# Optimization experiments

Measured on AMD Instinct MI355X. Metric: run time of the kernel, lower is better.

Reference implementation:

```python
import jax, jax.numpy as jnp
import numpy as np

B, T, W = 8, 4096, 1024          # batch, byte seq len, words per sequence
DB, DW = 64, 512                 # byte_embed_dim, word_embed_dim
NH = 2                           # highway layers per block
VOCAB = 264                      # 256 bytes + 4 + 4 specials
BPE_MARK, WORD_MARK = 4, 3       # bpe_mask_idx, word_mask_idx


def _make_seg_ids():
    # ragged word lengths in {3,4,5}, mean 4, summing to T per sequence
    rng = np.random.default_rng(0)
    seg = np.empty((B, T), np.int32)
    base = T // W
    for b in range(B):
        delta = np.zeros(W, np.int64)
        q = W // 4
        idx = rng.permutation(W)
        delta[idx[:q]] = 1
        delta[idx[q:2 * q]] = -1
        seg[b] = np.repeat(np.arange(W), base + delta)
    return jnp.asarray(seg)


def setup_inputs() -> dict:
    key = jax.random.key(0)
    ks = jax.random.split(key, 12)
    s = 0.05
    byte_tokens = jax.random.randint(ks[0], (B, T), 4, VOCAB)
    bpe_mask = jax.random.bernoulli(ks[1], 0.25, (B, T))
    word_mask = jax.random.bernoulli(ks[2], 0.05, (B, T))
    seg_ids = _make_seg_ids()
    tok_emb = (jax.random.normal(ks[3], (VOCAB, DB)) * s).at[0].set(0.0)  # padding_idx=0 row zeroed
    inp = {
        'byte_tokens': byte_tokens, 'bpe_mask': bpe_mask, 'word_mask': word_mask,
        'seg_ids': seg_ids, 'tok_emb': tok_emb,
        'conv0_w': jax.random.normal(ks[4], (3, DB, DW)) * s, 'conv0_b': jnp.zeros((DW,)),
        'hw0_wg': jax.random.normal(ks[5], (NH, DW, DW)) * s, 'hw0_bg': jnp.zeros((NH, DW)),
        'hw0_wh': jax.random.normal(ks[6], (NH, DW, DW)) * s, 'hw0_bh': jnp.zeros((NH, DW)),
        'conv1_w': jax.random.normal(ks[7], (3, DW, DW)) * s, 'conv1_b': jnp.zeros((DW,)),
        'hw1_wg': jax.random.normal(ks[8], (NH, DW, DW)) * s, 'hw1_bg': jnp.zeros((NH, DW)),
        'hw1_wh': jax.random.normal(ks[9], (NH, DW, DW)) * s, 'hw1_bh': jnp.zeros((NH, DW)),
        'proj_w': jax.random.normal(ks[10], (DW, DW)) * s, 'proj_b': jnp.zeros((DW,)),
    }
    return inp


def _conv_highway(x, cw, cb, wg, bg, wh, bh, residual):
    # 1D same-padded conv over sequence, optional residual, relu, then highways
    y = jax.lax.conv_general_dilated(x, cw, (1,), 'SAME',
                                     dimension_numbers=('NWC', 'WIO', 'NWC')) + cb
    if residual:
        y = y + x
    y = jax.nn.relu(y)
    for i in range(NH):
        g = jax.nn.sigmoid(y @ wg[i] + bg[i])
        h = jax.nn.relu(y @ wh[i] + bh[i])
        y = g * h + (1.0 - g) * y
    return y


def reference(byte_tokens, bpe_mask, word_mask, seg_ids, tok_emb,
              conv0_w, conv0_b, hw0_wg, hw0_bg, hw0_wh, hw0_bh,
              conv1_w, conv1_b, hw1_wg, hw1_bg, hw1_wh, hw1_bh,
              proj_w, proj_b):
    # byte embedding + marker embeddings (pad idx 0 -> zero row)
    x = (tok_emb[byte_tokens]
         + tok_emb[jnp.where(bpe_mask, BPE_MARK, 0)]
         + tok_emb[jnp.where(word_mask, WORD_MARK, 0)])          # [B,T,DB]
    x = _conv_highway(x, conv0_w, conv0_b, hw0_wg, hw0_bg, hw0_wh, hw0_bh, False)
    x = _conv_highway(x, conv1_w, conv1_b, hw1_wg, hw1_bg, hw1_wh, hw1_bh, True)
    # ragged per-word segment max over bytes (fused, replaces python loops)
    seg_max = jax.vmap(lambda xi, si: jax.ops.segment_max(xi, si, num_segments=W))
    x = seg_max(x, seg_ids)                                       # [B,W,DW]
    return x @ proj_w + proj_b
```

## Files before the change

kernel.cpp:

```cpp
#include <hip/hip_runtime.h>
#include <hip/hip_bf16.h>

using bf16 = __hip_bfloat16;
typedef __attribute__((ext_vector_type(8))) short s8v;
typedef __attribute__((ext_vector_type(4))) float f4v;

#define T_SEQ 4096
#define DWC 512

__device__ __forceinline__ float fin(float v) {
    return (v == v && fabsf(v) < 1e30f) ? v : 0.0f;
}
__device__ __forceinline__ float ldf(const void* p, size_t i, int f32) {
    return f32 ? ((const float*)p)[i] : __bfloat162float(((const bf16*)p)[i]);
}
__device__ __forceinline__ float b2f(short s) {
    unsigned u = ((unsigned)(unsigned short)s) << 16;
    return __builtin_bit_cast(float, u);
}
__device__ __forceinline__ short f2b(float v) {
    bf16 b = __float2bfloat16(v);
    return __builtin_bit_cast(short, b);
}
__device__ __forceinline__ uint4 ld16(const short* p) { return *(const uint4*)p; }

__device__ __forceinline__ void gl_lds16(const short* g, short* l) {
    __builtin_amdgcn_global_load_lds(
        (const __attribute__((address_space(1))) void*)g,
        (__attribute__((address_space(3))) void*)l, 16, 0, 0);
}

__device__ __forceinline__ void swz(int L, int G, int& bx, int& by) {
    int k8 = L & 7, sl = L >> 3;
    int gp = G >> 5;
    bx = sl & 3;
    by = k8 * gp + (sl >> 2);
}

__device__ __forceinline__ int swidx(int row, int ch) {
    return row * 32 + ((ch ^ ((row >> 1) & 3)) << 3);
}

__global__ __launch_bounds__(256) void diag_kernel(bf16* __restrict__ out, int n, float v)
{
    int i = blockIdx.x * 256 + threadIdx.x;
    if (i < n) out[i] = __float2bfloat16(i == 0 ? v : 0.0f);
}

__global__ __launch_bounds__(256) void detect_kernel(
    const int* __restrict__ tok, const unsigned char* __restrict__ bpe,
    const unsigned char* __restrict__ wm, const int* __restrict__ seg,
    const unsigned int* __restrict__ embw, int* __restrict__ flags)
{
    __shared__ int sh[5];
    int tid = threadIdx.x;
    if (tid < 5) sh[tid] = 0;
    __syncthreads();
    int bo = 0, bm = 0, wo = 0, wmid = 0;
    for (int i = tid; i < 16384; i += 256) {
        int odd = 2 * i + 1;
        if (bpe[odd]) bo = 1;
        if (wm[odd])  wo = 1;
        int mid = 8 * (i & 4095) + 4;
        if (bpe[mid]) bm = 1;
        if (wm[mid])  wmid = 1;
    }
    if (bo)   atomicOr(&sh[0], 1);
    if (bm)   atomicOr(&sh[1], 1);
    if (wo)   atomicOr(&sh[2], 1);
    if (wmid) atomicOr(&sh[3], 1);
    if (tid < 32 && embw[32 + tid] != 0u) atomicOr(&sh[4], 1);
    __syncthreads();
    if (tid == 0) {
        flags[0] = (tok[32767] != 0) ? 0 : 1;
        flags[1] = sh[0] ? 1 : (sh[1] ? 4 : 8);
        flags[2] = sh[2] ? 1 : (sh[3] ? 4 : 8);
        flags[3] = (seg[32767] != 0) ? 0 : 1;
        flags[4] = sh[4] ? 0 : 1;
    }
}

#define WB_TOTAL 3249664
#define EMB4_ELEMS (264 * 4 * 64)
__global__ __launch_bounds__(256) void convert_weights(
    const void* c0w, const void* c0b, const void* h0g, const void* h0bg,
    const void* h0h, const void* h0bh, const void* c1w, const void* c1b,
    const void* h1g, const void* h1bg, const void* h1h, const void* h1bh,
    const void* pw, const void* pb, const void* emb,
    const int* __restrict__ flags, short* __restrict__ WB)
{
    int f32 = flags[4];
    size_t i = (size_t)blockIdx.x * 256 + threadIdx.x;
    if (i >= WB_TOTAL + EMB4_ELEMS) return;
    if (i >= WB_TOTAL) {
        size_t o = i - WB_TOTAL;
        size_t t = o >> 8, v = (o >> 6) & 3, c = o & 63;
        float val = ldf(emb, t * 64 + c, f32);
        if (v & 1) val += ldf(emb, 4 * 64 + c, f32);
        if (v & 2) val += ldf(emb, 3 * 64 + c, f32);
        WB[i] = f2b(fin(val));
        return;
    }
    const void* src; size_t si;
    auto fraginv = [](size_t r, size_t& k, size_t& n) {
        size_t blk = r >> 9, w = r & 511;
        n = (blk >> 4) * 16 + ((w >> 3) & 15);
        k = (blk & 15) * 32 + (w >> 7) * 8 + (w & 7);
    };
    if (i < 98304)        { size_t n = i / 192, k = i % 192; src = c0w; si = k * 512 + n; }
    else if (i < 98816)   { src = c0b;  si = i - 98304; }
    else if (i < 623104)  { size_t o = i - 98816;  size_t l = o >> 18; size_t k, n;
                            fraginv(o & 262143, k, n);
                            src = h0g; si = (l << 18) + k * 512 + n; }
    else if (i < 624128)  { src = h0bg; si = i - 623104; }
    else if (i < 1148416) { size_t o = i - 624128; size_t l = o >> 18; size_t k, n;
                            fraginv(o & 262143, k, n);
                            src = h0h; si = (l << 18) + k * 512 + n; }
    else if (i < 1149440) { src = h0bh; si = i - 1148416; }
    else if (i < 1935872) { size_t o = i - 1149440; size_t n = o / 1536, k = o % 1536;
                            src = c1w; si = k * 512 + n; }
    else if (i < 1936384) { src = c1b;  si = i - 1935872; }
    else if (i < 2460672) { size_t o = i - 1936384; size_t l = o >> 18; size_t k, n;
                            fraginv(o & 262143, k, n);
                            src = h1g; si = (l << 18) + k * 512 + n; }
    else if (i < 2461696) { src = h1bg; si = i - 2460672; }
    else if (i < 2985984) { size_t o = i - 2461696; size_t l = o >> 18; size_t k, n;
                            fraginv(o & 262143, k, n);
                            src = h1h; si = (l << 18) + k * 512 + n; }
    else if (i < 2987008) { src = h1bh; si = i - 2985984; }
    else if (i < 3249152) { size_t o = i - 2987008; size_t n = o >> 9, k = o & 511;
                            src = pw; si = k * 512 + n; }
    else                  { src = pb;   si = i - 3249152; }
    WB[i] = f2b(ldf(src, si, f32));
}

__global__ __launch_bounds__(512) void conv0_mfma(
    const int* __restrict__ tok, const unsigned char* __restrict__ bpe,
    const unsigned char* __restrict__ wm, const short* __restrict__ emb4,
    const int* __restrict__ flags, const short* __restrict__ WT,
    const short* __restrict__ bias, short* __restrict__ Out)
{
    constexpr int K = 192;
    constexpr int NIT = 3;
    __shared__ __align__(16) short As[2][256 * 32];
    __shared__ __align__(16) short Bs[2][256 * 32];
    int bx, by;
    swz(blockIdx.x, gridDim.x, bx, by);
    const int bm = by * 128, bn = bx * 128;
    const int tid = threadIdx.x;
    const int wave = tid >> 6, lane = tid & 63;
    const int wmr = (wave >> 1) * 32, wnc = (wave & 1) * 64;
    const int q = lane >> 4, ln16 = lane & 15;
    const int sr = tid >> 2, sch = tid & 3;
    const int tt = (bm + sr) & (T_SEQ - 1);
    const int is64t = flags[0];
    const int wb = flags[1], ww = flags[2];
    const short* Bb = WT + (size_t)(bn + sr) * K + sch * 8;

    f4v acc[2][4] = {};
    uint4 rA0, rA1, rB0, rB1;
    const uint4 z4 = make_uint4(0, 0, 0, 0);

    auto loadA = [&](int tap, uint4& a0, uint4& a1) {
        int ts = tt + tap - 1;
        if ((unsigned)ts < (unsigned)T_SEQ) {
            int bt = bm + sr + tap - 1;
            int tk = is64t ? (int)((const long long*)tok)[bt] : tok[bt];
            tk = min(max(tk, 0), 263);
            int v = (bpe[(size_t)bt * wb] ? 1 : 0) | (wm[(size_t)bt * ww] ? 2 : 0);
            const short* row = emb4 + ((size_t)tk * 4 + v) * 64;
            a0 = ld16(row + sch * 8);
            a1 = ld16(row + 32 + sch * 8);
        } else { a0 = z4; a1 = z4; }
    };

    loadA(0, rA0, rA1);
    rB0 = ld16(Bb);
    rB1 = ld16(Bb + 32);
    *(uint4*)(&As[0][swidx(sr, sch)])       = rA0;
    *(uint4*)(&As[0][swidx(128 + sr, sch)]) = rA1;
    *(uint4*)(&Bs[0][swidx(sr, sch)])       = rB0;
    *(uint4*)(&Bs[0][swidx(128 + sr, sch)]) = rB1;
    __syncthreads();
    int p = 0;

    for (int it = 0; it < NIT; ++it) {
        const bool more = (it + 1 < NIT);
        if (more) {
            int kn = (it + 1) * 64;
            loadA(it + 1, rA0, rA1);
            rB0 = ld16(Bb + kn);
            rB1 = ld16(Bb + kn + 32);
        }
        #pragma unroll
        for (int ks = 0; ks < 2; ks++) {
            s8v af[2], bf[4];
            #pragma unroll
            for (int mi = 0; mi < 2; mi++)
                af[mi] = *(const s8v*)(&As[p][swidx(128 * ks + wmr + mi * 16 + ln16, q)]);
            #pragma unroll
            for (int ni = 0; ni < 4; ni++)
                bf[ni] = *(const s8v*)(&Bs[p][swidx(128 * ks + wnc + ni * 16 + ln16, q)]);
            #pragma unroll
            for (int mi = 0; mi < 2; mi++)
                #pragma unroll
                for (int ni = 0; ni < 4; ni++)
                    acc[mi][ni] = __builtin_amdgcn_mfma_f32_16x16x32_bf16(
                        af[mi], bf[ni], acc[mi][ni], 0, 0, 0);
        }
        if (more) {
            *(uint4*)(&As[p ^ 1][swidx(sr, sch)])       = rA0;
            *(uint4*)(&As[p ^ 1][swidx(128 + sr, sch)]) = rA1;
            *(uint4*)(&Bs[p ^ 1][swidx(sr, sch)])       = rB0;
            *(uint4*)(&Bs[p ^ 1][swidx(128 + sr, sch)]) = rB1;
            __syncthreads();
            p ^= 1;
        }
    }

    #pragma unroll
    for (int mi = 0; mi < 2; mi++)
        #pragma unroll
        for (int ni = 0; ni < 4; ni++) {
            int col = bn + wnc + ni * 16 + ln16;
            float bv = b2f(bias[col]);
            #pragma unroll
            for (int r = 0; r < 4; r++) {
                int orow = bm + wmr + mi * 16 + q * 4 + r;
                Out[(size_t)orow * DWC + col] =
                    f2b(fin(fmaxf(acc[mi][ni][r] + bv, 0.0f)));
            }
        }
}

__global__ __launch_bounds__(512) void conv1_mfma(
    const short* __restrict__ A, const short* __restrict__ WT,
    const short* __restrict__ bias, short* __restrict__ Out)
{
    constexpr int IC = 512;
    constexpr int K = 3 * IC;
    constexpr int NIT = K / 64;
    __shared__ __align__(16) short As[2][256 * 32];
    __shared__ __align__(16) short Bs[2][256 * 32];
    int bx, by;
    swz(blockIdx.x, gridDim.x, bx, by);
    const int bm = by * 128, bn = bx * 128;
    const int tid = threadIdx.x;
    const int wave = tid >> 6, lane = tid & 63;
    const int wmr = (wave >> 1) * 32, wnc = (wave & 1) * 64;
    const int q = lane >> 4, ln16 = lane & 15;
    const int sr = tid >> 2, sch = tid & 3;
    const int tt = (bm + sr) & (T_SEQ - 1);
    const short* Bb = WT + (size_t)(bn + sr) * K + sch * 8;

    f4v acc[2][4] = {};
    uint4 rA0, rA1, rB0, rB1;
    const uint4 z4 = make_uint4(0, 0, 0, 0);

    {
        int ts = tt - 1;
        bool ok = (ts >= 0 && ts < T_SEQ);
        const short* sa = A + (size_t)(bm + sr - 1) * IC + sch * 8;
        rA0 = ok ? ld16(sa) : z4;
        rA1 = ok ? ld16(sa + 32) : z4;
        rB0 = ld16(Bb);
        rB1 = ld16(Bb + 32);
    }
    *(uint4*)(&As[0][swidx(sr, sch)])       = rA0;
    *(uint4*)(&As[0][swidx(128 + sr, sch)]) = rA1;
    *(uint4*)(&Bs[0][swidx(sr, sch)])       = rB0;
    *(uint4*)(&Bs[0][swidx(128 + sr, sch)]) = rB1;
    __syncthreads();
    int p = 0;

    for (int it = 0; it < NIT; ++it) {
        const bool more = (it + 1 < NIT);
        if (more) {
            int kn = (it + 1) * 64;
            int tap = kn / IC, c0 = kn - tap * IC;
            int ts = tt + tap - 1;
            bool ok = (ts >= 0 && ts < T_SEQ);
            const short* sa = A + (size_t)(bm + sr + tap - 1) * IC + c0 + sch * 8;
            rA0 = ok ? ld16(sa) : z4;
            rA1 = ok ? ld16(sa + 32) : z4;
            rB0 = ld16(Bb + kn);
            rB1 = ld16(Bb + kn + 32);
        }
        #pragma unroll
        for (int ks = 0; ks < 2; ks++) {
            s8v af[2], bf[4];
            #pragma unroll
            for (int mi = 0; mi < 2; mi++)
                af[mi] = *(const s8v*)(&As[p][swidx(128 * ks + wmr + mi * 16 + ln16, q)]);
            #pragma unroll
            for (int ni = 0; ni < 4; ni++)
                bf[ni] = *(const s8v*)(&Bs[p][swidx(128 * ks + wnc + ni * 16 + ln16, q)]);
            #pragma unroll
            for (int mi = 0; mi < 2; mi++)
                #pragma unroll
                for (int ni = 0; ni < 4; ni++)
                    acc[mi][ni] = __builtin_amdgcn_mfma_f32_16x16x32_bf16(
                        af[mi], bf[ni], acc[mi][ni], 0, 0, 0);
        }
        if (more) {
            *(uint4*)(&As[p ^ 1][swidx(sr, sch)])       = rA0;
            *(uint4*)(&As[p ^ 1][swidx(128 + sr, sch)]) = rA1;
            *(uint4*)(&Bs[p ^ 1][swidx(sr, sch)])       = rB0;
            *(uint4*)(&Bs[p ^ 1][swidx(128 + sr, sch)]) = rB1;
            __syncthreads();
            p ^= 1;
        }
    }

    #pragma unroll
    for (int mi = 0; mi < 2; mi++)
        #pragma unroll
        for (int ni = 0; ni < 4; ni++) {
            int col = bn + wnc + ni * 16 + ln16;
            float bv = b2f(bias[col]);
            #pragma unroll
            for (int r = 0; r < 4; r++) {
                int orow = bm + wmr + mi * 16 + q * 4 + r;
                float v = acc[mi][ni][r] + bv + b2f(A[(size_t)orow * IC + col]);
                Out[(size_t)orow * DWC + col] = f2b(fin(fmaxf(v, 0.0f)));
            }
        }
}

__global__ __launch_bounds__(512, 4) void highway_mfma8(
    const short* __restrict__ Y, const short* __restrict__ WgF,
    const short* __restrict__ bg, const short* __restrict__ WhF,
    const short* __restrict__ bh, short* __restrict__ Out)
{
    constexpr int IC = DWC;
    constexpr int NIT = IC / 32;
    __shared__ __align__(16) short L[3][128 * 32];
    int bx, by;
    swz(blockIdx.x, gridDim.x, bx, by);
    const int bm = by * 128, bn = bx * 128;
    const int tid = threadIdx.x;
    const int wave = tid >> 6, lane = tid & 63;
    const int wmr = (wave >> 2) * 64;
    const int wnc = (wave & 3) * 32;
    const int q = lane >> 4, ln16 = lane & 15;

    const int rr = (wave << 4) + (lane >> 2);
    const int ch = (lane & 3) ^ ((rr >> 1) & 3);
    const short* gA = Y + (size_t)(bm + rr) * IC + ch * 8;
    const int wb1k = wave << 10;

    const short* Bg0 = WgF + (((size_t)(bn + wnc) >> 4) << 13) + (lane << 3);
    const short* Bh0 = WhF + (((size_t)(bn + wnc) >> 4) << 13) + (lane << 3);

    f4v accg[4][2] = {};
    f4v acch[4][2] = {};

    auto stage = [&](int pp, int kk) {
        gl_lds16(gA + kk, (short*)((char*)&L[pp][0] + wb1k));
    };

    stage(0, 0);
    stage(1, 32);
    asm volatile("s_waitcnt vmcnt(1)" ::: "memory");
    __builtin_amdgcn_s_barrier();
    int cur = 0, nn = 2;

    for (int it = 0; it < NIT; ++it) {
        const bool issue = (it + 2 < NIT);
        s8v bgf[2], bhf[2];
        #pragma unroll
        for (int ni = 0; ni < 2; ni++) {
            size_t fo = ((size_t)ni << 13) + ((size_t)it << 9);
            bgf[ni] = *(const s8v*)(Bg0 + fo);
            bhf[ni] = *(const s8v*)(Bh0 + fo);
        }
        if (issue) stage(nn, (it + 2) * 32);
        const short* Ap = &L[cur][0];
        s8v af[2];
        #pragma unroll
        for (int mh = 0; mh < 2; mh++) {
            #pragma unroll
            for (int mi = 0; mi < 2; mi++)
                af[mi] = *(const s8v*)(&Ap[swidx(wmr + mh * 32 + mi * 16 + ln16, q)]);
            #pragma unroll
            for (int mi = 0; mi < 2; mi++)
                #pragma unroll
                for (int ni = 0; ni < 2; ni++) {
                    accg[mh * 2 + mi][ni] = __builtin_amdgcn_mfma_f32_16x16x32_bf16(
                        af[mi], bgf[ni], accg[mh * 2 + mi][ni], 0, 0, 0);
                    acch[mh * 2 + mi][ni] = __builtin_amdgcn_mfma_f32_16x16x32_bf16(
                        af[mi], bhf[ni], acch[mh * 2 + mi][ni], 0, 0, 0);
                }
        }
        if (it + 1 < NIT) {
            if (issue) asm volatile("s_waitcnt vmcnt(1)" ::: "memory");
            else       asm volatile("s_waitcnt vmcnt(0)" ::: "memory");
            __builtin_amdgcn_s_barrier();
            cur = (cur == 2) ? 0 : cur + 1;
            nn  = (nn  == 2) ? 0 : nn  + 1;
        }
    }

    #pragma unroll
    for (int mi = 0; mi < 4; mi++)
        #pragma unroll
        for (int ni = 0; ni < 2; ni++) {
            int col = bn + wnc + ni * 16 + ln16;
            float bgv = b2f(bg[col]);
            float bhv = b2f(bh[col]);
            #pragma unroll
            for (int r = 0; r < 4; r++) {
                int orow = bm + wmr + mi * 16 + q * 4 + r;
                float g = 1.0f / (1.0f + expf(-(accg[mi][ni][r] + bgv)));
                float h = fmaxf(acch[mi][ni][r] + bhv, 0.0f);
                float yv = b2f(Y[(size_t)orow * DWC + col]);
                Out[(size_t)orow * DWC + col] = f2b(fin(g * h + (1.0f - g) * yv));
            }
        }
}

__global__ __launch_bounds__(512) void proj_mfma(
    const short* __restrict__ A, const short* __restrict__ WT,
    const short* __restrict__ bias, const int* __restrict__ flags,
    void* __restrict__ Out, int oroff)
{
    __shared__ __align__(16) short As[128 * 32];
    __shared__ __align__(16) short Bs[128 * 32];
    int bx, by;
    swz(blockIdx.x, gridDim.x, bx, by);
    const int bm = by * 128, bn = bx * 128;
    const int tid = threadIdx.x;
    const int wave = tid >> 6, lane = tid & 63;
    const int wmr = (wave >> 1) * 32, wnc = (wave & 1) * 64;
    const int q = lane >> 4, ln16 = lane & 15;
    const int sr = tid >> 2, sch = tid & 3;
    const int sw = swidx(sr, sch);
    const int f32 = flags[4];
    const short* A0 = A  + (size_t)(bm + sr) * DWC + sch * 8;
    const short* B0 = WT + (size_t)(bn + sr) * DWC + sch * 8;

    f4v acc[2][4] = {};
    uint4 rA = ld16(A0), rB = ld16(B0);

    for (int k0 = 0; k0 < DWC; k0 += 32) {
        *(uint4*)(&As[sw]) = rA;
        *(uint4*)(&Bs[sw]) = rB;
        __syncthreads();
        if (k0 + 32 < DWC) {
            int kn = k0 + 32;
            rA = ld16(A0 + kn); rB = ld16(B0 + kn);
        }
        s8v af[2], bf[4];
        #pragma unroll
        for (int mi = 0; mi < 2; mi++) af[mi] = *(const s8v*)(&As[swidx(wmr + mi * 16 + ln16, q)]);
        #pragma unroll
        for (int ni = 0; ni < 4; ni++) bf[ni] = *(const s8v*)(&Bs[swidx(wnc + ni * 16 + ln16, q)]);
        #pragma unroll
        for (int mi = 0; mi < 2; mi++)
            #pragma unroll
            for (int ni = 0; ni < 4; ni++)
                acc[mi][ni] = __builtin_amdgcn_mfma_f32_16x16x32_bf16(
                    af[mi], bf[ni], acc[mi][ni], 0, 0, 0);
        __syncthreads();
    }

    #pragma unroll
    for (int mi = 0; mi < 2; mi++)
        #pragma unroll
        for (int ni = 0; ni < 4; ni++) {
            int col = bn + wnc + ni * 16 + ln16;
            float bv = b2f(bias[col]);
            #pragma unroll
            for (int r = 0; r < 4; r++) {
                int orow = bm + wmr + mi * 16 + q * 4 + r;
                float v = fin(acc[mi][ni][r] + bv);
                size_t oi = (size_t)(oroff + orow) * DWC + col;
                if (f32) ((float*)Out)[oi] = v;
                else     ((bf16*)Out)[oi] = __float2bfloat16(v);
            }
        }
}

__global__ __launch_bounds__(256) void bounds_kernel(
    const int* __restrict__ seg, const int* __restrict__ flags,
    int* __restrict__ wstart, int* __restrict__ wend, int bt0)
{
    int il = blockIdx.x * 256 + threadIdx.x;
    int ig = bt0 + il;
    int is64 = flags[3];
    const long long* seg64 = (const long long*)seg;
    int t = il & (T_SEQ - 1);
    int bl = il >> 12;
    int s  = (is64 ? (int)seg64[ig] : seg[ig]) & 1023;
    int sp = (t == 0)         ? -1 : ((is64 ? (int)seg64[ig - 1] : seg[ig - 1]) & 1023);
    int sn = (t == T_SEQ - 1) ? -1 : ((is64 ? (int)seg64[ig + 1] : seg[ig + 1]) & 1023);
    int bw = (bl << 10) + s;
    if (sp != s) wstart[bw] = t;
    if (sn != s) wend[bw] = t;
}

__global__ __launch_bounds__(512) void segmax_kernel(
    const short* __restrict__ Y, const int* __restrict__ wstart,
    const int* __restrict__ wend, short* __restrict__ Out)
{
    int bw = blockIdx.x;
    int d = threadIdx.x;
    int bl = bw >> 10;
    int s = wstart[bw], e = wend[bw];
    s = min(max(s, 0), T_SEQ - 1);
    e = min(max(e, s), T_SEQ - 1);
    float m = b2f(Y[(size_t)((bl << 12) + s) * DWC + d]);
    for (int t = s + 1; t <= e; ++t)
        m = fmaxf(m, b2f(Y[(size_t)((bl << 12) + t) * DWC + d]));
    Out[(size_t)bw * DWC + d] = f2b(fin(m));
}

extern "C" void kernel_launch(void* const* d_in, const int* in_sizes, int n_in,
                              void* d_out, int out_size, void* d_ws, size_t ws_size,
                              hipStream_t stream)
{
    static const int expect[19] = {32768, 32768, 32768, 32768, 16896,
                                   98304, 512, 524288, 1024, 524288, 1024,
                                   786432, 512, 524288, 1024, 524288, 1024,
                                   262144, 512};
    int bad = -1;
    if (n_in < 19) bad = 31;
    else for (int i = 0; i < 19; i++) if (in_sizes[i] != expect[i]) { bad = i; break; }
    if (bad >= 0) {
        diag_kernel<<<dim3((out_size + 255) / 256), dim3(256), 0, stream>>>(
            (bf16*)d_out, out_size, 1e35f * (float)(1 + bad));
        return;
    }

    char* ws = (char*)d_ws;
    const size_t WBREG = 8ull << 20;
    short* WB    = (short*)ws;
    int*   flags = (int*)(ws + (7u << 20));
    const size_t perC = 8388608 + 8192 + 64;
    int C = 8;
    while (C > 1 && WBREG + (size_t)C * perC > ws_size) C >>= 1;
    if (WBREG + (size_t)C * perC > ws_size) {
        float ws_mib = (float)((double)ws_size / 1048576.0);
        diag_kernel<<<dim3((out_size + 255) / 256), dim3(256), 0, stream>>>(
            (bf16*)d_out, out_size, 1e30f * (16.0f + ws_mib));
        return;
    }

    const int*  byte_tokens = (const int*)d_in[0];
    const unsigned char* bpe_mask = (const unsigned char*)d_in[1];
    const unsigned char* word_mask = (const unsigned char*)d_in[2];
    const int*  seg_ids     = (const int*)d_in[3];
    const void* tok_emb = d_in[4];

    detect_kernel<<<dim3(1), dim3(256), 0, stream>>>(
        byte_tokens, bpe_mask, word_mask, seg_ids,
        (const unsigned int*)tok_emb, flags);

    convert_weights<<<dim3((WB_TOTAL + EMB4_ELEMS + 255) / 256), dim3(256), 0, stream>>>(
        d_in[5], d_in[6], d_in[7], d_in[8], d_in[9], d_in[10],
        d_in[11], d_in[12], d_in[13], d_in[14], d_in[15], d_in[16],
        d_in[17], d_in[18], tok_emb, flags, WB);

    short* c0wT = WB;            short* c0b  = WB + 98304;
    short* h0gF = WB + 98816;    short* h0bg = WB + 623104;
    short* h0hF = WB + 624128;   short* h0bh = WB + 1148416;
    short* c1wT = WB + 1149440;  short* c1b  = WB + 1935872;
    short* h1gF = WB + 1936384;  short* h1bg = WB + 2460672;
    short* h1hF = WB + 2461696;  short* h1bh = WB + 2985984;
    short* pwT  = WB + 2987008;  short* pb   = WB + 3249152;
    short* emb4 = WB + WB_TOTAL;
    const int LOFF = 262144, LBOFF = 512;

    for (int b0 = 0; b0 < 8; b0 += C) {
        const int rows  = C * T_SEQ;
        const int words = C * 1024;
        char*  chunk  = ws + WBREG;
        short* U      = (short*)chunk;
        short* V      = (short*)(chunk + (size_t)C * 4194304);
        int*   wstart = (int*)(chunk + (size_t)C * 8388608);
        int*   wend   = wstart + words;
        short* segout = U;

        dim3 gg(4 * (rows / 128));
        conv0_mfma<<<gg, dim3(512), 0, stream>>>(
            byte_tokens + (size_t)b0 * T_SEQ,
            bpe_mask, word_mask, emb4, flags, c0wT, c0b, U);

        highway_mfma8<<<gg, dim3(512), 0, stream>>>(U, h0gF, h0bg, h0hF, h0bh, V);
        highway_mfma8<<<gg, dim3(512), 0, stream>>>(V, h0gF + LOFF, h0bg + LBOFF,
                                                    h0hF + LOFF, h0bh + LBOFF, U);

        conv1_mfma<<<gg, dim3(512), 0, stream>>>(U, c1wT, c1b, V);

        highway_mfma8<<<gg, dim3(512), 0, stream>>>(V, h1gF, h1bg, h1hF, h1bh, U);
        highway_mfma8<<<gg, dim3(512), 0, stream>>>(U, h1gF + LOFF, h1bg + LBOFF,
                                                    h1hF + LOFF, h1bh + LBOFF, V);

        bounds_kernel<<<dim3(rows / 256), dim3(256), 0, stream>>>(
            seg_ids, flags, wstart, wend, b0 * T_SEQ);

        segmax_kernel<<<dim3(words), dim3(512), 0, stream>>>(V, wstart, wend, segout);

        proj_mfma<<<dim3(4 * (words / 128)), dim3(512), 0, stream>>>(
            segout, pwT, pb, flags, d_out, b0 * 1024);
    }
}
```

Baseline: 414.6 us.

## Tile weight conversion through LDS and stash highway residual tiles for coalesced output

```diff
diff --git a/kernel.cpp b/kernel.cpp
--- a/kernel.cpp
+++ b/kernel.cpp
@@ -82,56 +82,78 @@
 
 #define WB_TOTAL 3249664
 #define EMB4_ELEMS (264 * 4 * 64)
-__global__ __launch_bounds__(256) void convert_weights(
-    const void* c0w, const void* c0b, const void* h0g, const void* h0bg,
-    const void* h0h, const void* h0bh, const void* c1w, const void* c1b,
-    const void* h1g, const void* h1bg, const void* h1h, const void* h1bh,
-    const void* pw, const void* pb, const void* emb,
+
+__global__ __launch_bounds__(256) void convert_mats(
+    const void* c0w, const void* h0g, const void* h0h, const void* c1w,
+    const void* h1g, const void* h1h, const void* pw,
     const int* __restrict__ flags, short* __restrict__ WB)
 {
-    int f32 = flags[4];
-    size_t i = (size_t)blockIdx.x * 256 + threadIdx.x;
-    if (i >= WB_TOTAL + EMB4_ELEMS) return;
-    if (i >= WB_TOTAL) {
-        size_t o = i - WB_TOTAL;
-        size_t t = o >> 8, v = (o >> 6) & 3, c = o & 63;
-        float val = ldf(emb, t * 64 + c, f32);
+    __shared__ short lds[64][66];
+    const int f32 = flags[4];
+    const int bid = blockIdx.x;
+    const void* src; size_t soff, dbase; int K, t; bool frag;
+    if (bid < 24)       { src = c0w; soff = 0; dbase = 0;       K = 192;  frag = false; t = bid; }
+    else if (bid < 152) { int b = bid - 24;  int l = b >> 6; t = b & 63;
+                          src = h0g; soff = (size_t)l << 18; dbase = 98816   + ((size_t)l << 18); K = 512; frag = true; }
+    else if (bid < 280) { int b = bid - 152; int l = b >> 6; t = b & 63;
+                          src = h0h; soff = (size_t)l << 18; dbase = 624128  + ((size_t)l << 18); K = 512; frag = true; }
+    else if (bid < 472) { src = c1w; soff = 0; dbase = 1149440; K = 1536; frag = false; t = bid - 280; }
+    else if (bid < 600) { int b = bid - 472; int l = b >> 6; t = b & 63;
+                          src = h1g; soff = (size_t)l << 18; dbase = 1936384 + ((size_t)l << 18); K = 512; frag = true; }
+    else if (bid < 728) { int b = bid - 600; int l = b >> 6; t = b & 63;
+                          src = h1h; soff = (size_t)l << 18; dbase = 2461696 + ((size_t)l << 18); K = 512; frag = true; }
+    else                { src = pw;  soff = 0; dbase = 2987008; K = 512;  frag = false; t = bid - 728; }
+    const int k0 = (t >> 3) * 64, n0 = (t & 7) * 64;
+    const int tid = threadIdx.x;
+    #pragma unroll
+    for (int e = 0; e < 16; e++) {
+        int i = e * 256 + tid;
+        int r = i >> 6, c = i & 63;
+        lds[r][c] = f2b(ldf(src, soff + (size_t)(k0 + r) * 512 + n0 + c, f32));
+    }
+    __syncthreads();
+    if (!frag) {
+        #pragma unroll
+        for (int e = 0; e < 16; e++) {
+            int w = e * 256 + tid;
+            int rr = w >> 6, cc = w & 63;
+            WB[dbase + (size_t)(n0 + rr) * K + k0 + cc] = lds[cc][rr];
+        }
+    } else {
+        #pragma unroll
+        for (int e = 0; e < 16; e++) {
+            int w = e * 256 + tid;
+            int bi = w >> 9, wi = w & 511;
+            int nb = (n0 >> 4) + (bi >> 1), kb = (k0 >> 5) + (bi & 1);
+            int n = nb * 16 + ((wi >> 3) & 15);
+            int k = kb * 32 + ((wi >> 7) << 3) + (wi & 7);
+            WB[dbase + ((size_t)(nb * 16 + kb) << 9) + wi] = lds[k - k0][n - n0];
+        }
+    }
+}
+
+__global__ __launch_bounds__(256) void convert_small(
+    const void* c0b, const void* h0bg, const void* h0bh, const void* c1b,
+    const void* h1bg, const void* h1bh, const void* pb, const void* emb,
+    const int* __restrict__ flags, short* __restrict__ WB)
+{
+    const int f32 = flags[4];
+    int i = blockIdx.x * 256 + threadIdx.x;
+    if (i < 512)        WB[98304   + i]        = f2b(ldf(c0b,  i,        f32));
+    else if (i < 1536)  WB[623104  + (i - 512)]  = f2b(ldf(h0bg, i - 512,  f32));
+    else if (i < 2560)  WB[1148416 + (i - 1536)] = f2b(ldf(h0bh, i - 1536, f32));
+    else if (i < 3072)  WB[1935872 + (i - 2560)] = f2b(ldf(c1b,  i - 2560, f32));
+    else if (i < 4096)  WB[2460672 + (i - 3072)] = f2b(ldf(h1bg, i - 3072, f32));
+    else if (i < 5120)  WB[2985984 + (i - 4096)] = f2b(ldf(h1bh, i - 4096, f32));
+    else if (i < 5632)  WB[3249152 + (i - 5120)] = f2b(ldf(pb,   i - 5120, f32));
+    else if (i < 5632 + EMB4_ELEMS) {
+        size_t o = (size_t)(i - 5632);
+        size_t tt = o >> 8, v = (o >> 6) & 3, c = o & 63;
+        float val = ldf(emb, tt * 64 + c, f32);
         if (v & 1) val += ldf(emb, 4 * 64 + c, f32);
         if (v & 2) val += ldf(emb, 3 * 64 + c, f32);
-        WB[i] = f2b(fin(val));
-        return;
-    }
-    const void* src; size_t si;
-    auto fraginv = [](size_t r, size_t& k, size_t& n) {
-        size_t blk = r >> 9, w = r & 511;
-        n = (blk >> 4) * 16 + ((w >> 3) & 15);
-        k = (blk & 15) * 32 + (w >> 7) * 8 + (w & 7);
-    };
-    if (i < 98304)        { size_t n = i / 192, k = i % 192; src = c0w; si = k * 512 + n; }
-    else if (i < 98816)   { src = c0b;  si = i - 98304; }
-    else if (i < 623104)  { size_t o = i - 98816;  size_t l = o >> 18; size_t k, n;
-                            fraginv(o & 262143, k, n);
-                            src = h0g; si = (l << 18) + k * 512 + n; }
-    else if (i < 624128)  { src = h0bg; si = i - 623104; }
-    else if (i < 1148416) { size_t o = i - 624128; size_t l = o >> 18; size_t k, n;
-                            fraginv(o & 262143, k, n);
-                            src = h0h; si = (l << 18) + k * 512 + n; }
-    else if (i < 1149440) { src = h0bh; si = i - 1148416; }
-    else if (i < 1935872) { size_t o = i - 1149440; size_t n = o / 1536, k = o % 1536;
-                            src = c1w; si = k * 512 + n; }
-    else if (i < 1936384) { src = c1b;  si = i - 1935872; }
-    else if (i < 2460672) { size_t o = i - 1936384; size_t l = o >> 18; size_t k, n;
-                            fraginv(o & 262143, k, n);
-                            src = h1g; si = (l << 18) + k * 512 + n; }
-    else if (i < 2461696) { src = h1bg; si = i - 2460672; }
-    else if (i < 2985984) { size_t o = i - 2461696; size_t l = o >> 18; size_t k, n;
-                            fraginv(o & 262143, k, n);
-                            src = h1h; si = (l << 18) + k * 512 + n; }
-    else if (i < 2987008) { src = h1bh; si = i - 2985984; }
-    else if (i < 3249152) { size_t o = i - 2987008; size_t n = o >> 9, k = o & 511;
-                            src = pw; si = k * 512 + n; }
-    else                  { src = pb;   si = i - 3249152; }
-    WB[i] = f2b(ldf(src, si, f32));
+        WB[WB_TOTAL + o] = f2b(fin(val));
+    }
 }
 
 __global__ __launch_bounds__(512) void conv0_mfma(
@@ -334,10 +356,11 @@
 {
     constexpr int IC = DWC;
     constexpr int NIT = IC / 32;
-    __shared__ __align__(16) short L[3][128 * 32];
+    __shared__ __align__(16) short L[7][128 * 32];
     int bx, by;
     swz(blockIdx.x, gridDim.x, bx, by);
     const int bm = by * 128, bn = bx * 128;
+    const int s0 = bn >> 5;
     const int tid = threadIdx.x;
     const int wave = tid >> 6, lane = tid & 63;
     const int wmr = (wave >> 2) * 64;
@@ -355,15 +378,19 @@
     f4v accg[4][2] = {};
     f4v acch[4][2] = {};
 
+    auto bufOf = [&](int t) -> int {
+        if (t >= s0 && t < s0 + 4) return 3 + (t - s0);
+        int np = (t < s0) ? t : (t - 4);
+        return np - (np / 3) * 3;
+    };
     auto stage = [&](int pp, int kk) {
         gl_lds16(gA + kk, (short*)((char*)&L[pp][0] + wb1k));
     };
 
-    stage(0, 0);
-    stage(1, 32);
+    stage(bufOf(0), 0);
+    stage(bufOf(1), 32);
     asm volatile("s_waitcnt vmcnt(1)" ::: "memory");
     __builtin_amdgcn_s_barrier();
-    int cur = 0, nn = 2;
 
     for (int it = 0; it < NIT; ++it) {
         const bool issue = (it + 2 < NIT);
@@ -374,8 +401,8 @@
             bgf[ni] = *(const s8v*)(Bg0 + fo);
             bhf[ni] = *(const s8v*)(Bh0 + fo);
         }
-        if (issue) stage(nn, (it + 2) * 32);
-        const short* Ap = &L[cur][0];
+        if (issue) stage(bufOf(it + 2), (it + 2) * 32);
+        const short* Ap = &L[bufOf(it)][0];
         s8v af[2];
         #pragma unroll
         for (int mh = 0; mh < 2; mh++) {
@@ -396,27 +423,40 @@
             if (issue) asm volatile("s_waitcnt vmcnt(1)" ::: "memory");
             else       asm volatile("s_waitcnt vmcnt(0)" ::: "memory");
             __builtin_amdgcn_s_barrier();
-            cur = (cur == 2) ? 0 : cur + 1;
-            nn  = (nn  == 2) ? 0 : nn  + 1;
-        }
-    }
+        }
+    }
+
+    __builtin_amdgcn_s_barrier();
 
     #pragma unroll
     for (int mi = 0; mi < 4; mi++)
         #pragma unroll
         for (int ni = 0; ni < 2; ni++) {
-            int col = bn + wnc + ni * 16 + ln16;
+            int c = wnc + ni * 16 + ln16;
+            int col = bn + c;
             float bgv = b2f(bg[col]);
             float bhv = b2f(bh[col]);
+            short* stash = &L[3 + (c >> 5)][0];
+            int k = c & 31;
             #pragma unroll
             for (int r = 0; r < 4; r++) {
-                int orow = bm + wmr + mi * 16 + q * 4 + r;
+                int row = wmr + mi * 16 + q * 4 + r;
+                int si = row * 32 + ((((k >> 3) ^ ((row >> 1) & 3))) << 3) + (k & 7);
                 float g = 1.0f / (1.0f + expf(-(accg[mi][ni][r] + bgv)));
                 float h = fmaxf(acch[mi][ni][r] + bhv, 0.0f);
-                float yv = b2f(Y[(size_t)orow * DWC + col]);
-                Out[(size_t)orow * DWC + col] = f2b(fin(g * h + (1.0f - g) * yv));
+                float yv = b2f(stash[si]);
+                stash[si] = f2b(fin(g * h + (1.0f - g) * yv));
             }
         }
+    __syncthreads();
+
+    const int orow = tid >> 2, och = tid & 3;
+    const int chc = och ^ ((orow >> 1) & 3);
+    #pragma unroll
+    for (int j = 0; j < 4; j++) {
+        uint4 v = *(const uint4*)(&L[3 + j][orow * 32 + (och << 3)]);
+        *(uint4*)(Out + (size_t)(bm + orow) * DWC + bn + j * 32 + chc * 8) = v;
+    }
 }
 
 __global__ __launch_bounds__(512) void proj_mfma(
@@ -556,10 +596,12 @@
         byte_tokens, bpe_mask, word_mask, seg_ids,
         (const unsigned int*)tok_emb, flags);
 
-    convert_weights<<<dim3((WB_TOTAL + EMB4_ELEMS + 255) / 256), dim3(256), 0, stream>>>(
-        d_in[5], d_in[6], d_in[7], d_in[8], d_in[9], d_in[10],
-        d_in[11], d_in[12], d_in[13], d_in[14], d_in[15], d_in[16],
-        d_in[17], d_in[18], tok_emb, flags, WB);
+    convert_mats<<<dim3(792), dim3(256), 0, stream>>>(
+        d_in[5], d_in[7], d_in[9], d_in[11], d_in[13], d_in[15], d_in[17],
+        flags, WB);
+    convert_small<<<dim3((5632 + EMB4_ELEMS + 255) / 256), dim3(256), 0, stream>>>(
+        d_in[6], d_in[8], d_in[10], d_in[12], d_in[14], d_in[16], d_in[18],
+        tok_emb, flags, WB);
 
     short* c0wT = WB;            short* c0b  = WB + 98304;
     short* h0gF = WB + 98816;    short* h0bg = WB + 623104;
```

Result: slower. 435.9 us (+5.1%).
